# Kernel optimization log

Measured on AMD Instinct MI355X. Metric: run time of the kernel, lower is better.

The kernel has to match this reference:

```python
import jax, jax.numpy as jnp
import numpy as np

NUM_HEAD = 8
LN_EPS = 1e-5


def setup_inputs() -> dict:
    key = jax.random.key(0)
    ks = jax.random.split(key, 10)
    Nd = 32768          # num destination nodes
    E = 524288          # num edges (= num extra src nodes, TGL convention)
    Dn, De, Dt, Do = 128, 128, 128, 128

    h = jax.random.normal(ks[0], (Nd + E, Dn), dtype=jnp.float32)
    f = jax.random.normal(ks[1], (E, De), dtype=jnp.float32)
    dt = jax.random.uniform(ks[2], (E,), dtype=jnp.float32) * 100.0
    dst_idx = jax.random.randint(ks[3], (E,), 0, Nd, dtype=jnp.int32)

    # TimeEncode params (init = 1/10^linspace(0,9,dim), bias 0; both learnable)
    freq = jnp.asarray(1.0 / 10.0 ** np.linspace(0, 9, Dt, dtype=np.float32))
    time_bias = jnp.zeros((Dt,), dtype=jnp.float32)

    def lin(k, out_d, in_d):
        s = 1.0 / np.sqrt(in_d)
        return jax.random.uniform(k, (out_d, in_d), jnp.float32, -s, s)

    Wq = lin(ks[4], Do, Dn + Dt)
    Wk = lin(ks[5], Do, Dn + De + Dt)
    Wv = lin(ks[6], Do, Dn + De + Dt)
    Wout = lin(ks[7], Do, Dn + Do)
    bq = jnp.zeros((Do,), jnp.float32)
    bk = jnp.zeros((Do,), jnp.float32)
    bv = jnp.zeros((Do,), jnp.float32)
    bout = jnp.zeros((Do,), jnp.float32)
    ln_gamma = jnp.ones((Do,), jnp.float32)
    ln_beta = jnp.zeros((Do,), jnp.float32)

    return {"h": h, "f": f, "dt": dt, "dst_idx": dst_idx,
            "freq": freq, "time_bias": time_bias,
            "Wq": Wq, "bq": bq, "Wk": Wk, "bk": bk, "Wv": Wv, "bv": bv,
            "Wout": Wout, "bout": bout, "ln_gamma": ln_gamma, "ln_beta": ln_beta}


def reference(h, f, dt, dst_idx, freq, time_bias, Wq, bq, Wk, bk, Wv, bv,
              Wout, bout, ln_gamma, ln_beta):
    E = dt.shape[0]
    Nd = h.shape[0] - E          # srcdata['h'][:Nd] are dst nodes, rest map 1:1 to edges
    Do = Wq.shape[0]
    H = NUM_HEAD

    h_dst = h[:Nd]               # [Nd, Dn]
    h_src = h[Nd:]               # [E, Dn], source node of edge i is Nd+i

    # TimeEncode: cos(t * freq + bias)
    time_feat = jnp.cos(dt[:, None] * freq[None, :] + time_bias)      # [E, Dt]
    zero_time_feat = jnp.broadcast_to(jnp.cos(time_bias), (Nd, freq.shape[0]))

    # Q over dst nodes, gathered per edge
    Q_in = jnp.concatenate([h_dst, zero_time_feat], axis=1)           # [Nd, Dn+Dt]
    Q_nodes = Q_in @ Wq.T + bq                                        # [Nd, Do]
    Q = Q_nodes[dst_idx]                                              # [E, Do]

    # K/V over per-edge (src node, edge feat, time feat)
    KV_in = jnp.concatenate([h_src, f, time_feat], axis=1)            # [E, Dn+De+Dt]
    K = KV_in @ Wk.T + bk
    V = KV_in @ Wv.T + bv

    Qh = Q.reshape(E, H, -1)
    Kh = K.reshape(E, H, -1)
    Vh = V.reshape(E, H, -1)

    logits = jax.nn.leaky_relu(jnp.sum(Qh * Kh, axis=2), 0.2)         # [E, H]

    # edge_softmax: softmax over edges sharing the same destination node
    seg_max = jax.ops.segment_max(logits, dst_idx, num_segments=Nd)   # [Nd, H]
    ex = jnp.exp(logits - seg_max[dst_idx])
    seg_sum = jax.ops.segment_sum(ex, dst_idx, num_segments=Nd)       # [Nd, H]
    att = ex / seg_sum[dst_idx]                                       # [E, H]

    Vw = (Vh * att[:, :, None]).reshape(E, Do)                        # [E, Do]
    agg = jax.ops.segment_sum(Vw, dst_idx, num_segments=Nd)           # [Nd, Do]

    rst = jnp.concatenate([agg, h_dst], axis=1) @ Wout.T + bout       # [Nd, Do]
    rst = jax.nn.relu(rst)                                            # dropout=0 (eval)

    mu = jnp.mean(rst, axis=-1, keepdims=True)
    var = jnp.var(rst, axis=-1, keepdims=True)
    return (rst - mu) / jnp.sqrt(var + LN_EPS) * ln_gamma + ln_beta
```

## Files before the change

kernel.cpp:

```cpp
#include <hip/hip_runtime.h>
#include <cstdint>
#include <cstddef>

#define LN_EPS 1e-5f

typedef __attribute__((ext_vector_type(8))) short short8;
typedef __attribute__((ext_vector_type(4))) float f32x4;

static __device__ __forceinline__ unsigned short f2bf(float x) {
    union { float f; unsigned u; } v; v.f = x;
    unsigned r = v.u + 0x7FFFu + ((v.u >> 16) & 1u);
    return (unsigned short)(r >> 16);
}
static __device__ __forceinline__ float bf2f(unsigned short b) {
    union { unsigned u; float f; } v; v.u = ((unsigned)b) << 16;
    return v.f;
}

__global__ void prep_kernel(const float* __restrict__ Wq, const float* __restrict__ bq,
                            const float* __restrict__ Wk, const float* __restrict__ Wv,
                            const float* __restrict__ Wout, const float* __restrict__ tb,
                            unsigned short* __restrict__ wkv, unsigned short* __restrict__ wq,
                            unsigned short* __restrict__ wout, float* __restrict__ qbias) {
    int tid = blockIdx.x * blockDim.x + threadIdx.x;
    if (tid < 256 * 384) {
        int o = tid / 384, k = tid % 384;
        float w = (o < 128) ? Wk[o * 384 + k] : Wv[(o - 128) * 384 + k];
        wkv[tid] = f2bf(w);
    }
    if (tid < 128 * 128) {
        int o = tid / 128, i = tid % 128;
        wq[tid] = f2bf(Wq[o * 256 + i]);
    }
    if (tid < 128 * 256) {
        wout[tid] = f2bf(Wout[tid]);
    }
    if (tid < 128) {
        float s = bq[tid];
        for (int t = 0; t < 128; ++t) s += cosf(tb[t]) * Wq[tid * 256 + 128 + t];
        qbias[tid] = s;
    }
}

__launch_bounds__(256)
__global__ void gemm_kv_kernel(const float* __restrict__ h, const float* __restrict__ f,
                               const float* __restrict__ dt, const float* __restrict__ freq,
                               const float* __restrict__ tb,
                               const unsigned short* __restrict__ wkv,
                               const float* __restrict__ bk, const float* __restrict__ bv,
                               unsigned short* __restrict__ Kb, unsigned short* __restrict__ Vb,
                               int Nd, int E) {
    __shared__ unsigned short ldsA[4 * 12 * 64 * 8];
    const int tid = threadIdx.x;
    const long e_base = (long)blockIdx.x * 64;

    for (int g = tid; g < 64 * 96; g += 256) {
        int r  = g / 96;
        int c4 = (g % 96) * 4;
        long e = e_base + r; if (e >= E) e = E - 1;
        float v0, v1, v2, v3;
        if (c4 < 128) {
            float4 x = *(const float4*)(h + ((long)Nd + e) * 128 + c4);
            v0 = x.x; v1 = x.y; v2 = x.z; v3 = x.w;
        } else if (c4 < 256) {
            float4 x = *(const float4*)(f + e * 128 + (c4 - 128));
            v0 = x.x; v1 = x.y; v2 = x.z; v3 = x.w;
        } else {
            int t = c4 - 256;
            float d = dt[e];
            v0 = __cosf(fmaf(d, freq[t + 0], tb[t + 0]));
            v1 = __cosf(fmaf(d, freq[t + 1], tb[t + 1]));
            v2 = __cosf(fmaf(d, freq[t + 2], tb[t + 2]));
            v3 = __cosf(fmaf(d, freq[t + 3], tb[t + 3]));
        }
        int mt   = r >> 4;
        int lane = (r & 15) | (((c4 >> 3) & 3) << 4);
        int ks   = c4 >> 5;
        int base = ((mt * 12 + ks) * 64 + lane) * 8 + (c4 & 7);
        *(unsigned*)&ldsA[base]     = (unsigned)f2bf(v0) | ((unsigned)f2bf(v1) << 16);
        *(unsigned*)&ldsA[base + 2] = (unsigned)f2bf(v2) | ((unsigned)f2bf(v3) << 16);
    }
    __syncthreads();

    const int w = tid >> 6, l = tid & 63, ln = l & 15, lq = l >> 4;
    f32x4 acc[4][4] = {};
    for (int ks = 0; ks < 12; ++ks) {
        short8 bfr[4], afr[4];
        #pragma unroll
        for (int nt = 0; nt < 4; ++nt) {
            int row = w * 64 + nt * 16 + ln;
            bfr[nt] = *(const short8*)(wkv + row * 384 + ks * 32 + lq * 8);
        }
        #pragma unroll
        for (int mt = 0; mt < 4; ++mt)
            afr[mt] = *(const short8*)&ldsA[((mt * 12 + ks) * 64 + l) * 8];
        #pragma unroll
        for (int mt = 0; mt < 4; ++mt)
            #pragma unroll
            for (int nt = 0; nt < 4; ++nt)
                acc[mt][nt] = __builtin_amdgcn_mfma_f32_16x16x32_bf16(
                    afr[mt], bfr[nt], acc[mt][nt], 0, 0, 0);
    }
    #pragma unroll
    for (int mt = 0; mt < 4; ++mt) {
        #pragma unroll
        for (int nt = 0; nt < 4; ++nt) {
            int cg = w * 64 + nt * 16 + ln;
            float bias = (cg < 128) ? bk[cg] : bv[cg - 128];
            #pragma unroll
            for (int rg = 0; rg < 4; ++rg) {
                long e = e_base + mt * 16 + lq * 4 + rg;
                if (e >= E) continue;
                unsigned short ob = f2bf(acc[mt][nt][rg] + bias);
                if (cg < 128) Kb[e * 128 + cg]         = ob;
                else          Vb[e * 128 + (cg - 128)] = ob;
            }
        }
    }
}

__launch_bounds__(256)
__global__ void gemm_node_kernel(const float* __restrict__ src0, const float* __restrict__ src1,
                                 const unsigned short* __restrict__ W, const float* __restrict__ bias,
                                 float* __restrict__ out, int M, int ksteps, int do_relu) {
    __shared__ unsigned short ldsA[4 * 8 * 64 * 8];
    const int tid = threadIdx.x;
    const long m_base = (long)blockIdx.x * 64;
    const int Kd = ksteps * 32;
    const int g4 = Kd / 4;

    for (int g = tid; g < 64 * g4; g += 256) {
        int r  = g / g4;
        int c4 = (g % g4) * 4;
        long m = m_base + r; if (m >= M) m = M - 1;
        float4 x = (c4 < 128) ? *(const float4*)(src0 + m * 128 + c4)
                              : *(const float4*)(src1 + m * 128 + (c4 - 128));
        int lane = (r & 15) | (((c4 >> 3) & 3) << 4);
        int base = (((r >> 4) * ksteps + (c4 >> 5)) * 64 + lane) * 8 + (c4 & 7);
        *(unsigned*)&ldsA[base]     = (unsigned)f2bf(x.x) | ((unsigned)f2bf(x.y) << 16);
        *(unsigned*)&ldsA[base + 2] = (unsigned)f2bf(x.z) | ((unsigned)f2bf(x.w) << 16);
    }
    __syncthreads();

    const int w = tid >> 6, l = tid & 63, ln = l & 15, lq = l >> 4;
    f32x4 acc[4][2] = {};
    for (int ks = 0; ks < ksteps; ++ks) {
        short8 bfr[2], afr[4];
        #pragma unroll
        for (int nt = 0; nt < 2; ++nt) {
            int row = w * 32 + nt * 16 + ln;
            bfr[nt] = *(const short8*)(W + row * Kd + ks * 32 + lq * 8);
        }
        #pragma unroll
        for (int mt = 0; mt < 4; ++mt)
            afr[mt] = *(const short8*)&ldsA[((mt * ksteps + ks) * 64 + l) * 8];
        #pragma unroll
        for (int mt = 0; mt < 4; ++mt)
            #pragma unroll
            for (int nt = 0; nt < 2; ++nt)
                acc[mt][nt] = __builtin_amdgcn_mfma_f32_16x16x32_bf16(
                    afr[mt], bfr[nt], acc[mt][nt], 0, 0, 0);
    }
    #pragma unroll
    for (int mt = 0; mt < 4; ++mt) {
        #pragma unroll
        for (int nt = 0; nt < 2; ++nt) {
            int cg = w * 32 + nt * 16 + ln;
            float b = bias[cg];
            #pragma unroll
            for (int rg = 0; rg < 4; ++rg) {
                long m = m_base + mt * 16 + lq * 4 + rg;
                if (m >= M) continue;
                float val = acc[mt][nt][rg] + b;
                if (do_relu) val = fmaxf(val, 0.f);
                out[m * 128 + cg] = val;
            }
        }
    }
}

__global__ void hist_kernel(const int* __restrict__ dst, int* __restrict__ counts, int E) {
    int e = blockIdx.x * blockDim.x + threadIdx.x;
    if (e < E) atomicAdd(&counts[dst[e]], 1);
}

__global__ void scan_kernel(const int* __restrict__ counts, int* __restrict__ offsets,
                            int* __restrict__ cursor, int Nd) {
    __shared__ int sdata[1024];
    int t = threadIdx.x;
    int C = (Nd + 1023) / 1024;
    int b0 = t * C;
    int s = 0;
    for (int i = 0; i < C; ++i) { int idx = b0 + i; if (idx < Nd) s += counts[idx]; }
    sdata[t] = s;
    __syncthreads();
    for (int off = 1; off < 1024; off <<= 1) {
        int v = (t >= off) ? sdata[t - off] : 0;
        __syncthreads();
        sdata[t] += v;
        __syncthreads();
    }
    int run = sdata[t] - s;
    for (int i = 0; i < C; ++i) {
        int idx = b0 + i;
        if (idx < Nd) { offsets[idx] = run; cursor[idx] = run; run += counts[idx]; }
    }
}

__global__ void scatter_kernel(const int* __restrict__ dst, int* __restrict__ cursor,
                               int* __restrict__ order, int E) {
    int e = blockIdx.x * blockDim.x + threadIdx.x;
    if (e < E) { int pos = atomicAdd(&cursor[dst[e]], 1); order[pos] = e; }
}

__launch_bounds__(128)
__global__ void attn_kernel(const float* __restrict__ Q, const unsigned short* __restrict__ Kb,
                            const unsigned short* __restrict__ Vb,
                            const int* __restrict__ order, const int* __restrict__ offsets,
                            const int* __restrict__ counts, float* __restrict__ agg) {
    const int d = blockIdx.x;
    const int t = threadIdx.x;
    const int beg = offsets[d];
    const int n   = counts[d];
    const float q = Q[(long)d * 128 + t];

    float m = -3.0e38f, lsum = 0.f, acc = 0.f;
    float kk = 0.f, vv = 0.f;
    if (n > 0) {
        int e0 = order[beg];
        kk = bf2f(Kb[(long)e0 * 128 + t]);
        vv = bf2f(Vb[(long)e0 * 128 + t]);
    }
    for (int i = 0; i < n; ++i) {
        float ck = kk, cv = vv;
        if (i + 1 < n) {
            int e2 = order[beg + i + 1];
            kk = bf2f(Kb[(long)e2 * 128 + t]);
            vv = bf2f(Vb[(long)e2 * 128 + t]);
        }
        float p = q * ck;
        p += __shfl_xor(p, 1, 16);
        p += __shfl_xor(p, 2, 16);
        p += __shfl_xor(p, 4, 16);
        p += __shfl_xor(p, 8, 16);
        float logit = (p > 0.f) ? p : 0.2f * p;
        float mn = fmaxf(m, logit);
        float sc = __expf(m - mn);
        float pe = __expf(logit - mn);
        lsum = lsum * sc + pe;
        acc  = acc * sc + pe * cv;
        m = mn;
    }
    agg[(long)d * 128 + t] = (n > 0) ? acc / lsum : 0.f;
}

__launch_bounds__(256)
__global__ void ln_kernel(const float* __restrict__ rst, const float* __restrict__ gamma,
                          const float* __restrict__ beta, float* __restrict__ out, int Nd) {
    int wave = threadIdx.x >> 6;
    int lane = threadIdx.x & 63;
    long row = (long)blockIdx.x * 4 + wave;
    if (row >= Nd) return;
    float x0 = rst[row * 128 + lane];
    float x1 = rst[row * 128 + 64 + lane];
    float s = x0 + x1, sq = x0 * x0 + x1 * x1;
    #pragma unroll
    for (int off = 32; off >= 1; off >>= 1) {
        s  += __shfl_xor(s, off, 64);
        sq += __shfl_xor(sq, off, 64);
    }
    float mean = s * (1.f / 128.f);
    float var  = sq * (1.f / 128.f) - mean * mean;
    float rstd = rsqrtf(var + LN_EPS);
    out[row * 128 + lane]      = (x0 - mean) * rstd * gamma[lane]      + beta[lane];
    out[row * 128 + 64 + lane] = (x1 - mean) * rstd * gamma[lane + 64] + beta[lane + 64];
}

extern "C" void kernel_launch(void* const* d_in, const int* in_sizes, int n_in,
                              void* d_out, int out_size, void* d_ws, size_t ws_size,
                              hipStream_t stream) {
    const float* h    = (const float*)d_in[0];
    const float* f    = (const float*)d_in[1];
    const float* dt   = (const float*)d_in[2];
    const int*   dst  = (const int*)d_in[3];
    const float* freq = (const float*)d_in[4];
    const float* tb   = (const float*)d_in[5];
    const float* Wq   = (const float*)d_in[6];
    const float* bq   = (const float*)d_in[7];
    const float* Wk   = (const float*)d_in[8];
    const float* bk   = (const float*)d_in[9];
    const float* Wv   = (const float*)d_in[10];
    const float* bv   = (const float*)d_in[11];
    const float* Wout = (const float*)d_in[12];
    const float* bout = (const float*)d_in[13];
    const float* gamma= (const float*)d_in[14];
    const float* beta = (const float*)d_in[15];

    const int E  = in_sizes[2];
    const int Nd = in_sizes[0] / 128 - E;

    char* ws = (char*)d_ws;
    size_t off = 0;
    auto alloc = [&](size_t b) {
        off = (off + 255) & ~(size_t)255;
        char* p = ws + off; off += b; return p;
    };
    unsigned short* wkv   = (unsigned short*)alloc(256 * 384 * 2);
    unsigned short* wq    = (unsigned short*)alloc(128 * 128 * 2);
    unsigned short* wout  = (unsigned short*)alloc(128 * 256 * 2);
    float*          qbias = (float*)alloc(128 * 4);
    float*          Q     = (float*)alloc((size_t)Nd * 128 * 4);
    unsigned short* Kb    = (unsigned short*)alloc((size_t)E * 128 * 2);
    unsigned short* Vb    = (unsigned short*)alloc((size_t)E * 128 * 2);
    float*          agg   = (float*)alloc((size_t)Nd * 128 * 4);
    int*            counts= (int*)alloc((size_t)Nd * 4);
    int*            offs  = (int*)alloc((size_t)Nd * 4);
    int*            cursor= (int*)alloc((size_t)Nd * 4);
    int*            order = (int*)alloc((size_t)E * 4);
    float*          rst   = (float*)Kb;

    hipMemsetAsync(counts, 0, (size_t)Nd * 4, stream);
    prep_kernel<<<(256 * 384 + 255) / 256, 256, 0, stream>>>(Wq, bq, Wk, Wv, Wout, tb,
                                                             wkv, wq, wout, qbias);
    hist_kernel<<<(E + 255) / 256, 256, 0, stream>>>(dst, counts, E);
    scan_kernel<<<1, 1024, 0, stream>>>(counts, offs, cursor, Nd);
    scatter_kernel<<<(E + 255) / 256, 256, 0, stream>>>(dst, cursor, order, E);
    gemm_node_kernel<<<(Nd + 63) / 64, 256, 0, stream>>>(h, nullptr, wq, qbias, Q, Nd, 4, 0);
    gemm_kv_kernel<<<(E + 63) / 64, 256, 0, stream>>>(h, f, dt, freq, tb, wkv, bk, bv,
                                                      Kb, Vb, Nd, E);
    attn_kernel<<<Nd, 128, 0, stream>>>(Q, Kb, Vb, order, offs, counts, agg);
    gemm_node_kernel<<<(Nd + 63) / 64, 256, 0, stream>>>(agg, h, wout, bout, rst, Nd, 8, 1);
    ln_kernel<<<(Nd + 3) / 4, 256, 0, stream>>>(rst, gamma, beta, (float*)d_out, Nd);
}
```

Baseline: 1.314 ms.

## Pipeline KV GEMM with async global-to-LDS double buffering and vectorized epilogues

Rewrites the K/V projection kernel to use 128-row tiles with 512 threads. The h and f inputs are streamed as fp32 through double-buffered, XOR-swizzled LDS using direct global-to-LDS loads, so the next chunk's load overlaps MFMA work on the current one. Conversion to bf16 now happens at fragment-read time, and the time-encoding features are computed in registers instead of being staged. MFMA operands are swapped so each lane holds 4 consecutive output columns, which allows packed vector stores in both GEMM epilogues and uses a hardware bf16x2 conversion. The cost is more LDS per block (64 KB of fp32 buffers) and extra register pressure.

```diff
diff --git a/kernel.cpp b/kernel.cpp
--- a/kernel.cpp
+++ b/kernel.cpp
@@ -1,4 +1,5 @@
 #include <hip/hip_runtime.h>
+#include <hip/hip_bf16.h>
 #include <cstdint>
 #include <cstddef>
 
@@ -15,6 +16,11 @@
 static __device__ __forceinline__ float bf2f(unsigned short b) {
     union { unsigned u; float f; } v; v.u = ((unsigned)b) << 16;
     return v.f;
+}
+static __device__ __forceinline__ unsigned cvt2(float lo, float hi) {
+    float2 p; p.x = lo; p.y = hi;
+    __hip_bfloat162 h = __float22bfloat162_rn(p);
+    unsigned u; __builtin_memcpy(&u, &h, 4); return u;
 }
 
 __global__ void prep_kernel(const float* __restrict__ Wq, const float* __restrict__ bq,
@@ -42,7 +48,7 @@
     }
 }
 
-__launch_bounds__(256)
+__launch_bounds__(512, 4)
 __global__ void gemm_kv_kernel(const float* __restrict__ h, const float* __restrict__ f,
                                const float* __restrict__ dt, const float* __restrict__ freq,
                                const float* __restrict__ tb,
@@ -50,71 +56,118 @@
                                const float* __restrict__ bk, const float* __restrict__ bv,
                                unsigned short* __restrict__ Kb, unsigned short* __restrict__ Vb,
                                int Nd, int E) {
-    __shared__ unsigned short ldsA[4 * 12 * 64 * 8];
+    __shared__ __align__(1024) float ldsA[2][8192];
     const int tid = threadIdx.x;
-    const long e_base = (long)blockIdx.x * 64;
-
-    for (int g = tid; g < 64 * 96; g += 256) {
-        int r  = g / 96;
-        int c4 = (g % 96) * 4;
-        long e = e_base + r; if (e >= E) e = E - 1;
-        float v0, v1, v2, v3;
-        if (c4 < 128) {
-            float4 x = *(const float4*)(h + ((long)Nd + e) * 128 + c4);
-            v0 = x.x; v1 = x.y; v2 = x.z; v3 = x.w;
-        } else if (c4 < 256) {
-            float4 x = *(const float4*)(f + e * 128 + (c4 - 128));
-            v0 = x.x; v1 = x.y; v2 = x.z; v3 = x.w;
-        } else {
-            int t = c4 - 256;
-            float d = dt[e];
-            v0 = __cosf(fmaf(d, freq[t + 0], tb[t + 0]));
-            v1 = __cosf(fmaf(d, freq[t + 1], tb[t + 1]));
-            v2 = __cosf(fmaf(d, freq[t + 2], tb[t + 2]));
-            v3 = __cosf(fmaf(d, freq[t + 3], tb[t + 3]));
-        }
-        int mt   = r >> 4;
-        int lane = (r & 15) | (((c4 >> 3) & 3) << 4);
-        int ks   = c4 >> 5;
-        int base = ((mt * 12 + ks) * 64 + lane) * 8 + (c4 & 7);
-        *(unsigned*)&ldsA[base]     = (unsigned)f2bf(v0) | ((unsigned)f2bf(v1) << 16);
-        *(unsigned*)&ldsA[base + 2] = (unsigned)f2bf(v2) | ((unsigned)f2bf(v3) << 16);
-    }
+    const int w  = tid >> 6, l = tid & 63, ln = l & 15, lq = l >> 4;
+    const int wm = w >> 2, wn = w & 3;
+    const long e_base = (long)blockIdx.x * 128;
+
+    auto stage = [&](int c, int buf) {
+        #pragma unroll
+        for (int i = 0; i < 4; ++i) {
+            int inst = w * 4 + i;
+            int a    = inst * 1024 + l * 16;
+            int row  = a >> 8;
+            int colb = (a & 255) ^ ((row & 7) << 5);
+            long er  = e_base + row; if (er >= E) er = E - 1;
+            const float* g = (c < 2) ? h + ((long)Nd + er) * 128 + c * 64 + (colb >> 2)
+                                     : f + er * 128 + (c - 2) * 64 + (colb >> 2);
+            __builtin_amdgcn_global_load_lds(
+                (const __attribute__((address_space(1))) void*)g,
+                (__attribute__((address_space(3))) void*)&ldsA[buf][inst * 256],
+                16, 0, 0);
+        }
+    };
+
+    stage(0, 0);
+    f32x4 acc[4][4] = {};
     __syncthreads();
 
-    const int w = tid >> 6, l = tid & 63, ln = l & 15, lq = l >> 4;
-    f32x4 acc[4][4] = {};
-    for (int ks = 0; ks < 12; ++ks) {
-        short8 bfr[4], afr[4];
+    int buf = 0;
+    #pragma unroll
+    for (int c = 0; c < 4; ++c) {
+        short8 wfr[2][4];
+        #pragma unroll
+        for (int ksl = 0; ksl < 2; ++ksl)
+            #pragma unroll
+            for (int nt = 0; nt < 4; ++nt) {
+                int o = wn * 64 + nt * 16 + ln;
+                wfr[ksl][nt] = *(const short8*)(wkv + o * 384 + c * 64 + ksl * 32 + lq * 8);
+            }
+        if (c < 3) stage(c + 1, buf ^ 1);
+        #pragma unroll
+        for (int ksl = 0; ksl < 2; ++ksl) {
+            #pragma unroll
+            for (int mt = 0; mt < 4; ++mt) {
+                int row = wm * 64 + mt * 16 + ln;
+                int swz = ((ksl * 32 + lq * 8) << 2) ^ ((row & 7) << 5);
+                const float* p = &ldsA[buf][row * 64 + (swz >> 2)];
+                float4 x0 = *(const float4*)p;
+                float4 x1 = *(const float4*)(p + 4);
+                union { short8 s; unsigned u[4]; } v;
+                v.u[0] = cvt2(x0.x, x0.y); v.u[1] = cvt2(x0.z, x0.w);
+                v.u[2] = cvt2(x1.x, x1.y); v.u[3] = cvt2(x1.z, x1.w);
+                #pragma unroll
+                for (int nt = 0; nt < 4; ++nt)
+                    acc[mt][nt] = __builtin_amdgcn_mfma_f32_16x16x32_bf16(
+                        wfr[ksl][nt], v.s, acc[mt][nt], 0, 0, 0);
+            }
+        }
+        __syncthreads();
+        buf ^= 1;
+    }
+
+    float dval[4];
+    #pragma unroll
+    for (int mt = 0; mt < 4; ++mt) {
+        long e = e_base + wm * 64 + mt * 16 + ln;
+        if (e >= E) e = E - 1;
+        dval[mt] = dt[e];
+    }
+    #pragma unroll
+    for (int ks = 0; ks < 4; ++ks) {
+        int t0 = ks * 32 + lq * 8;
+        short8 wfr[4];
         #pragma unroll
         for (int nt = 0; nt < 4; ++nt) {
-            int row = w * 64 + nt * 16 + ln;
-            bfr[nt] = *(const short8*)(wkv + row * 384 + ks * 32 + lq * 8);
-        }
-        #pragma unroll
-        for (int mt = 0; mt < 4; ++mt)
-            afr[mt] = *(const short8*)&ldsA[((mt * 12 + ks) * 64 + l) * 8];
-        #pragma unroll
-        for (int mt = 0; mt < 4; ++mt)
+            int o = wn * 64 + nt * 16 + ln;
+            wfr[nt] = *(const short8*)(wkv + o * 384 + 256 + ks * 32 + lq * 8);
+        }
+        float4 f0 = *(const float4*)(freq + t0);
+        float4 f1 = *(const float4*)(freq + t0 + 4);
+        float4 b0 = *(const float4*)(tb + t0);
+        float4 b1 = *(const float4*)(tb + t0 + 4);
+        #pragma unroll
+        for (int mt = 0; mt < 4; ++mt) {
+            float d = dval[mt];
+            union { short8 s; unsigned u[4]; } v;
+            v.u[0] = cvt2(__cosf(fmaf(d, f0.x, b0.x)), __cosf(fmaf(d, f0.y, b0.y)));
+            v.u[1] = cvt2(__cosf(fmaf(d, f0.z, b0.z)), __cosf(fmaf(d, f0.w, b0.w)));
+            v.u[2] = cvt2(__cosf(fmaf(d, f1.x, b1.x)), __cosf(fmaf(d, f1.y, b1.y)));
+            v.u[3] = cvt2(__cosf(fmaf(d, f1.z, b1.z)), __cosf(fmaf(d, f1.w, b1.w)));
             #pragma unroll
             for (int nt = 0; nt < 4; ++nt)
                 acc[mt][nt] = __builtin_amdgcn_mfma_f32_16x16x32_bf16(
-                    afr[mt], bfr[nt], acc[mt][nt], 0, 0, 0);
-    }
-    #pragma unroll
-    for (int mt = 0; mt < 4; ++mt) {
-        #pragma unroll
-        for (int nt = 0; nt < 4; ++nt) {
-            int cg = w * 64 + nt * 16 + ln;
-            float bias = (cg < 128) ? bk[cg] : bv[cg - 128];
-            #pragma unroll
-            for (int rg = 0; rg < 4; ++rg) {
-                long e = e_base + mt * 16 + lq * 4 + rg;
-                if (e >= E) continue;
-                unsigned short ob = f2bf(acc[mt][nt][rg] + bias);
-                if (cg < 128) Kb[e * 128 + cg]         = ob;
-                else          Vb[e * 128 + (cg - 128)] = ob;
-            }
+                    wfr[nt], v.s, acc[mt][nt], 0, 0, 0);
+        }
+    }
+
+    #pragma unroll
+    for (int nt = 0; nt < 4; ++nt) {
+        int o0 = wn * 64 + nt * 16 + lq * 4;
+        const float* bsrc = (o0 < 128) ? (bk + o0) : (bv + (o0 - 128));
+        float4 b4 = *(const float4*)bsrc;
+        #pragma unroll
+        for (int mt = 0; mt < 4; ++mt) {
+            long e = e_base + wm * 64 + mt * 16 + ln;
+            if (e >= E) continue;
+            f32x4 a = acc[mt][nt];
+            uint2 u;
+            u.x = cvt2(a[0] + b4.x, a[1] + b4.y);
+            u.y = cvt2(a[2] + b4.z, a[3] + b4.w);
+            unsigned short* dst = (o0 < 128) ? (Kb + e * 128 + o0)
+                                             : (Vb + e * 128 + (o0 - 128));
+            *(uint2*)dst = u;
         }
     }
 }
@@ -137,44 +190,46 @@
                               : *(const float4*)(src1 + m * 128 + (c4 - 128));
         int lane = (r & 15) | (((c4 >> 3) & 3) << 4);
         int base = (((r >> 4) * ksteps + (c4 >> 5)) * 64 + lane) * 8 + (c4 & 7);
-        *(unsigned*)&ldsA[base]     = (unsigned)f2bf(x.x) | ((unsigned)f2bf(x.y) << 16);
-        *(unsigned*)&ldsA[base + 2] = (unsigned)f2bf(x.z) | ((unsigned)f2bf(x.w) << 16);
+        *(unsigned*)&ldsA[base]     = cvt2(x.x, x.y);
+        *(unsigned*)&ldsA[base + 2] = cvt2(x.z, x.w);
     }
     __syncthreads();
 
     const int w = tid >> 6, l = tid & 63, ln = l & 15, lq = l >> 4;
     f32x4 acc[4][2] = {};
     for (int ks = 0; ks < ksteps; ++ks) {
-        short8 bfr[2], afr[4];
+        short8 bfr[2];
         #pragma unroll
         for (int nt = 0; nt < 2; ++nt) {
             int row = w * 32 + nt * 16 + ln;
             bfr[nt] = *(const short8*)(W + row * Kd + ks * 32 + lq * 8);
         }
         #pragma unroll
-        for (int mt = 0; mt < 4; ++mt)
-            afr[mt] = *(const short8*)&ldsA[((mt * ksteps + ks) * 64 + l) * 8];
-        #pragma unroll
-        for (int mt = 0; mt < 4; ++mt)
+        for (int mt = 0; mt < 4; ++mt) {
+            short8 afr = *(const short8*)&ldsA[((mt * ksteps + ks) * 64 + l) * 8];
             #pragma unroll
             for (int nt = 0; nt < 2; ++nt)
                 acc[mt][nt] = __builtin_amdgcn_mfma_f32_16x16x32_bf16(
-                    afr[mt], bfr[nt], acc[mt][nt], 0, 0, 0);
-    }
-    #pragma unroll
-    for (int mt = 0; mt < 4; ++mt) {
-        #pragma unroll
-        for (int nt = 0; nt < 2; ++nt) {
-            int cg = w * 32 + nt * 16 + ln;
-            float b = bias[cg];
-            #pragma unroll
-            for (int rg = 0; rg < 4; ++rg) {
-                long m = m_base + mt * 16 + lq * 4 + rg;
-                if (m >= M) continue;
-                float val = acc[mt][nt][rg] + b;
-                if (do_relu) val = fmaxf(val, 0.f);
-                out[m * 128 + cg] = val;
+                    bfr[nt], afr, acc[mt][nt], 0, 0, 0);
+        }
+    }
+    #pragma unroll
+    for (int nt = 0; nt < 2; ++nt) {
+        int o0 = w * 32 + nt * 16 + lq * 4;
+        float4 b4 = *(const float4*)(bias + o0);
+        #pragma unroll
+        for (int mt = 0; mt < 4; ++mt) {
+            long m = m_base + mt * 16 + ln;
+            if (m >= M) continue;
+            f32x4 a = acc[mt][nt];
+            float4 o;
+            o.x = a[0] + b4.x; o.y = a[1] + b4.y;
+            o.z = a[2] + b4.z; o.w = a[3] + b4.w;
+            if (do_relu) {
+                o.x = fmaxf(o.x, 0.f); o.y = fmaxf(o.y, 0.f);
+                o.z = fmaxf(o.z, 0.f); o.w = fmaxf(o.w, 0.f);
             }
+            *(float4*)(out + m * 128 + o0) = o;
         }
     }
 }
@@ -326,8 +381,8 @@
     scan_kernel<<<1, 1024, 0, stream>>>(counts, offs, cursor, Nd);
     scatter_kernel<<<(E + 255) / 256, 256, 0, stream>>>(dst, cursor, order, E);
     gemm_node_kernel<<<(Nd + 63) / 64, 256, 0, stream>>>(h, nullptr, wq, qbias, Q, Nd, 4, 0);
-    gemm_kv_kernel<<<(E + 63) / 64, 256, 0, stream>>>(h, f, dt, freq, tb, wkv, bk, bv,
-                                                      Kb, Vb, Nd, E);
+    gemm_kv_kernel<<<(E + 127) / 128, 512, 0, stream>>>(h, f, dt, freq, tb, wkv, bk, bv,
+                                                        Kb, Vb, Nd, E);
     attn_kernel<<<Nd, 128, 0, stream>>>(Q, Kb, Vb, order, offs, counts, agg);
     gemm_node_kernel<<<(Nd + 63) / 64, 256, 0, stream>>>(agg, h, wout, bout, rst, Nd, 8, 1);
     ln_kernel<<<(Nd + 3) / 4, 256, 0, stream>>>(rst, gamma, beta, (float*)d_out, Nd);
```

Measured after the change: 1.208 ms. -8.1%, faster.
